# Optimization experiments

Hardware: AMD Instinct MI355X
Metric: run time of the kernel (lower is better)

## Reference

```python
import jax, jax.numpy as jnp
import numpy as np

B, T, F, G, H, N, C = 32, 64, 32, 32, 256, 20000, 32
EPS = 1e-5


def setup_inputs() -> dict:
    key = jax.random.key(0)
    ks = jax.random.split(key, 24)
    s = 0.05
    d = {}
    d["data_feats"] = jax.random.normal(ks[0], (B, T, F), jnp.float32)
    d["gat_output"] = jax.random.normal(ks[1], (B, N, G), jnp.float32)
    d["row_ids"] = jax.random.randint(ks[2], (B, T), 0, 2 * N, jnp.int32)
    d["node_ids"] = jax.random.randint(ks[3], (N,), 0, 2 * N, jnp.int32)
    # shared LSTM (2 layers): layer0 input F+G, layer1 input H; b = b_ih + b_hh fused
    d["shared_Wih0"] = jax.random.normal(ks[4], (4 * H, F + G)) * s
    d["shared_Whh0"] = jax.random.normal(ks[5], (4 * H, H)) * s
    d["shared_b0"] = jax.random.normal(ks[6], (4 * H,)) * s
    d["shared_Wih1"] = jax.random.normal(ks[7], (4 * H, H)) * s
    d["shared_Whh1"] = jax.random.normal(ks[8], (4 * H, H)) * s
    d["shared_b1"] = jax.random.normal(ks[9], (4 * H,)) * s
    # act/time/timeR LSTMs stacked on leading axis 3, each 2 layers of [4H,H]
    d["heads_Wih"] = jax.random.normal(ks[10], (3, 2, 4 * H, H)) * s
    d["heads_Whh"] = jax.random.normal(ks[11], (3, 2, 4 * H, H)) * s
    d["heads_b"] = jax.random.normal(ks[12], (3, 2, 4 * H)) * s
    d["bn_gnn_g"] = jnp.ones((G,), jnp.float32)
    d["bn_gnn_b"] = jnp.zeros((G,), jnp.float32)
    d["bn_shared_g"] = jnp.ones((H,), jnp.float32)
    d["bn_shared_b"] = jnp.zeros((H,), jnp.float32)
    d["heads_bn_g"] = jnp.ones((3, H), jnp.float32)
    d["heads_bn_b"] = jnp.zeros((3, H), jnp.float32)
    d["fc_act_W"] = jax.random.normal(ks[13], (C, H)) * s
    d["fc_act_b"] = jnp.zeros((C,), jnp.float32)
    d["fc_time_W"] = jax.random.normal(ks[14], (1, H)) * s
    d["fc_time_b"] = jnp.zeros((1,), jnp.float32)
    d["fc_timeR_W"] = jax.random.normal(ks[15], (1, H)) * s
    d["fc_timeR_b"] = jnp.zeros((1,), jnp.float32)
    return d


def batchnorm(x, gamma, beta):
    # BatchNorm1d training-mode: stats over (batch, length) per channel; x: [B, L, C]
    mean = jnp.mean(x, axis=(0, 1))
    var = jnp.var(x, axis=(0, 1))
    return (x - mean) * (gamma / jnp.sqrt(var + EPS)) + beta


def lstm_layer(x, Wih, Whh, b):
    # x: [B, T, Din]; PyTorch gate order i, f, g, o
    xp = jnp.einsum("btf,gf->btg", x, Wih) + b  # [B, T, 4H]
    h = Whh.shape[1]
    init = (jnp.zeros((x.shape[0], h), x.dtype), jnp.zeros((x.shape[0], h), x.dtype))

    def step(carry, xt):
        hprev, cprev = carry
        gates = xt + hprev @ Whh.T
        i, f, g, o = jnp.split(gates, 4, axis=-1)
        c = jax.nn.sigmoid(f) * cprev + jax.nn.sigmoid(i) * jnp.tanh(g)
        hnew = jax.nn.sigmoid(o) * jnp.tanh(c)
        return (hnew, c), hnew

    _, hs = jax.lax.scan(step, init, jnp.swapaxes(xp, 0, 1))
    return jnp.swapaxes(hs, 0, 1)  # [B, T, H]


def reference(data_feats, gat_output, row_ids, node_ids,
              shared_Wih0, shared_Whh0, shared_b0,
              shared_Wih1, shared_Whh1, shared_b1,
              heads_Wih, heads_Whh, heads_b,
              bn_gnn_g, bn_gnn_b, bn_shared_g, bn_shared_b,
              heads_bn_g, heads_bn_b,
              fc_act_W, fc_act_b, fc_time_W, fc_time_b, fc_timeR_W, fc_timeR_b):
    # --- graph branch: BN over GAT output, value-match lookup + gather ---
    gat_norm = batchnorm(gat_output, bn_gnn_g, bn_gnn_b)  # [B, N, G]
    eq = row_ids[:, :, None] == node_ids[None, None, :]   # [B, T, N]
    idx = jnp.argmax(eq, axis=-1)                          # first matching index
    found = jnp.any(eq, axis=-1)
    gathered = jnp.take_along_axis(gat_norm, idx[:, :, None], axis=1)  # [B, T, G]
    matched = jnp.where(found[:, :, None], gathered, 0.0)
    lstm_in = jnp.concatenate([data_feats, matched], axis=-1)  # [B, T, F+G]

    # --- shared 2-layer LSTM + BN (dropout off / eval) ---
    shared = lstm_layer(lstm_in, shared_Wih0, shared_Whh0, shared_b0)
    shared = lstm_layer(shared, shared_Wih1, shared_Whh1, shared_b1)
    shared = batchnorm(shared, bn_shared_g, bn_shared_b)

    # --- act / time / timeR head LSTMs (vmapped over the 3 heads) + BN ---
    def head(Wih, Whh, b, g, bb):
        hh = lstm_layer(shared, Wih[0], Whh[0], b[0])
        hh = lstm_layer(hh, Wih[1], Whh[1], b[1])
        return batchnorm(hh, g, bb)

    heads = jax.vmap(head)(heads_Wih, heads_Whh, heads_b, heads_bn_g, heads_bn_b)
    last = heads[:, :, -1, :]  # [3, B, H]

    act = jax.nn.softmax(last[0] @ fc_act_W.T + fc_act_b, axis=1)
    time = last[1] @ fc_time_W.T + fc_time_b
    timeR = last[2] @ fc_timeR_W.T + fc_timeR_b
    return act, time, timeR
```

## Files before the change

kernel.cpp:

```cpp
#include <hip/hip_runtime.h>
#include <hip/hip_fp16.h>
#include <math.h>

#define Bn 32
#define Tn 64
#define Fdim 32
#define Gdim 32
#define Hdim 256
#define Ndim 20000
#define Cdim 32
#define G4 1024
#define BT 2048
#define EPSc 1e-5f

__device__ __forceinline__ float sigmoidf_(float x){ return 1.0f/(1.0f + __expf(-x)); }
__device__ __forceinline__ float tanhf_(float x){ return 2.0f/(1.0f+__expf(-2.0f*x)) - 1.0f; }

typedef _Float16 h2t __attribute__((ext_vector_type(2)));

__device__ __forceinline__ float fdot2_(unsigned w, unsigned h, float acc){
#if defined(__has_builtin) && __has_builtin(__builtin_amdgcn_fdot2)
  return __builtin_amdgcn_fdot2(__builtin_bit_cast(h2t, w), __builtin_bit_cast(h2t, h), acc, false);
#else
  h2t a = __builtin_bit_cast(h2t, w), b = __builtin_bit_cast(h2t, h);
  acc = fmaf((float)a.x, (float)b.x, acc);
  return fmaf((float)a.y, (float)b.y, acc);
#endif
}

__global__ void init_kernel(float* ws){
  int i = blockIdx.x*256 + threadIdx.x;
  if (i < 2112) ws[i] = 0.0f;
  int* table = (int*)(ws + 2112);
  if (i < 40000) table[i] = 0x7fffffff;
}

__global__ void bn_stats_kernel(const float* __restrict__ gat, float* __restrict__ sums){
  __shared__ float ss[256], sq[256];
  int tid = threadIdx.x;
  int idx = blockIdx.x*256 + tid;
  int stride = gridDim.x*256;
  const int total = Bn*Ndim*Gdim;
  float s=0.f,q=0.f;
  for (int i=idx; i<total; i+=stride){ float v = gat[i]; s+=v; q+=v*v; }
  ss[tid]=s; sq[tid]=q; __syncthreads();
  for (int off=128; off>=32; off>>=1){
    if(tid<off){ ss[tid]+=ss[tid+off]; sq[tid]+=sq[tid+off]; }
    __syncthreads();
  }
  if (tid<32){ atomicAdd(&sums[tid], ss[tid]); atomicAdd(&sums[32+tid], sq[tid]); }
}

__global__ void table_kernel(const int* __restrict__ node_ids, int* __restrict__ table){
  int i = blockIdx.x*256 + threadIdx.x;
  if (i < Ndim) atomicMin(&table[node_ids[i]], i);
}

__global__ void build_input_kernel(const float* __restrict__ feats, const float* __restrict__ gat,
    const int* __restrict__ row_ids, const int* __restrict__ table, const float* __restrict__ sums,
    const float* __restrict__ bng, const float* __restrict__ bnb, float* __restrict__ out){
  int gt = blockIdx.x*256 + threadIdx.x;
  int pos = gt >> 6; int lane = gt & 63;
  float v;
  if (lane < 32){
    v = feats[pos*Fdim + lane];
  } else {
    int g = lane - 32;
    int r = row_ids[pos];
    int idx = table[r];
    if (idx < Ndim){
      int b = pos / Tn;
      float x = gat[(b*Ndim + idx)*Gdim + g];
      const float cnt = (float)(Bn*Ndim);
      float mean = sums[g]/cnt;
      float var  = sums[32+g]/cnt - mean*mean;
      v = (x-mean)*bng[g]*rsqrtf(var+EPSc) + bnb[g];
    } else v = 0.0f;
  }
  out[gt] = v;
}

struct TArgs { const float* src[8]; float* dst[8]; int K[8]; };
__global__ void transpose_kernel(TArgs a){
  __shared__ float tile[32][33];
  int mat = blockIdx.y;
  int K = a.K[mat];
  int tc = blockIdx.x & 7; int tr = blockIdx.x >> 3;
  if (tc*32 >= K) return;
  const float* src = a.src[mat]; float* dst = a.dst[mat];
  int tx = threadIdx.x; int ty = threadIdx.y;
  int r0 = tr*32, c0 = tc*32;
  #pragma unroll
  for (int i=0;i<4;i++){ int r = ty + i*8; tile[r][tx] = src[(r0+r)*K + c0+tx]; }
  __syncthreads();
  #pragma unroll
  for (int i=0;i<4;i++){ int r = ty + i*8; dst[(c0 + r)*G4 + r0 + tx] = tile[tx][r]; }
}

struct PkArgs { const float* src[8]; };
__global__ void pack_kernel(PkArgs a, unsigned* __restrict__ dst){
  int gid = blockIdx.x*256 + threadIdx.x;
  int m = gid >> 17;
  int rem = gid & 0x1FFFF;
  int q = rem & 3;
  int t2 = (rem >> 2) & 1023;
  int ci = rem >> 12;
  int c = ci >> 3, i = ci & 7;
  int j = t2 & 255, kq = t2 >> 8;
  int r = 4*j + c;
  int k = kq*64 + 8*i + 2*q;
  const float* W = a.src[m];
  float lo = W[r*256 + k], hi = W[r*256 + k + 1];
  unsigned ulo = (unsigned)__half_as_ushort(__float2half(lo));
  unsigned uhi = (unsigned)__half_as_ushort(__float2half(hi));
  dst[gid] = ulo | (uhi << 16);
}

struct PArgs { const float* x[3]; const float* wt[3]; const float* bias[3]; float* out[3]; int K; };
__global__ __launch_bounds__(256) void proj_kernel(PArgs a){
  int hd = blockIdx.z;
  int j  = blockIdx.y*256 + threadIdx.x;
  int m0 = blockIdx.x*4;
  const float* x  = a.x[hd];
  const float* wt = a.wt[hd];
  int K = a.K;
  float bv = a.bias[hd][j];
  float acc0=bv, acc1=bv, acc2=bv, acc3=bv;
  const float* x0 = x + m0*K;
  #pragma unroll 4
  for (int k=0;k<K;k++){
    float w = wt[k*G4 + j];
    acc0 = fmaf(x0[k],     w, acc0);
    acc1 = fmaf(x0[K+k],   w, acc1);
    acc2 = fmaf(x0[2*K+k], w, acc2);
    acc3 = fmaf(x0[3*K+k], w, acc3);
  }
  float* out = a.out[hd] + m0*G4 + j;
  out[0]=acc0; out[G4]=acc1; out[2*G4]=acc2; out[3*G4]=acc3;
}

struct RArgs { const float* xp[3]; const unsigned* wt[3]; float* out[3]; };
__global__ __launch_bounds__(1024,1) void rec_kernel(RArgs a){
  extern __shared__ float lds[];
  unsigned* lw   = (unsigned*)lds;
  float*    part = lds + 32768;
  unsigned* hp   = (unsigned*)(lds + 36864);
  int b = blockIdx.x, hd = blockIdx.y, tid = threadIdx.x;
  int j = tid & 255, kq = tid >> 8;
  const float* xp = a.xp[hd] + (size_t)b*Tn*G4;
  const unsigned* wt = a.wt[hd];
  float* out = a.out[hd] + (size_t)b*Tn*Hdim;

  unsigned w[96];
  #pragma unroll
  for (int c=0;c<4;c++){
    #pragma unroll
    for (int i=0;i<6;i++){
      uint4 v = *(const uint4*)(wt + ((c*8+i)*1024 + tid)*4);
      w[(c*6+i)*4+0]=v.x; w[(c*6+i)*4+1]=v.y; w[(c*6+i)*4+2]=v.z; w[(c*6+i)*4+3]=v.w;
    }
    #pragma unroll
    for (int i=6;i<8;i++){
      uint4 v = *(const uint4*)(wt + ((c*8+i)*1024 + tid)*4);
      *(uint4*)(lw + ((c*2+(i-6))*1024 + tid)*4) = v;
    }
  }
  float cst = 0.0f;
  if (tid < 128){ hp[tid] = 0u; hp[128+tid] = 0u; }
  __syncthreads();

  int p = 0;
  for (int t=0; t<Tn; t++){
    float ac0, ac1, ac2, ac3;
    if (kq == 0){
      float4 xv = *(const float4*)(xp + t*G4 + 4*j);
      ac0=xv.x; ac1=xv.y; ac2=xv.z; ac3=xv.w;
    } else { ac0=0.f; ac1=0.f; ac2=0.f; ac3=0.f; }
    const unsigned* hrow = hp + p*128 + kq*32;
    #pragma unroll
    for (int ic=0; ic<6; ic++){
      uint4 hv = *(const uint4*)(hrow + 4*ic);
      ac0=fdot2_(w[0*24+ic*4+0],hv.x,ac0); ac0=fdot2_(w[0*24+ic*4+1],hv.y,ac0);
      ac0=fdot2_(w[0*24+ic*4+2],hv.z,ac0); ac0=fdot2_(w[0*24+ic*4+3],hv.w,ac0);
      ac1=fdot2_(w[1*24+ic*4+0],hv.x,ac1); ac1=fdot2_(w[1*24+ic*4+1],hv.y,ac1);
      ac1=fdot2_(w[1*24+ic*4+2],hv.z,ac1); ac1=fdot2_(w[1*24+ic*4+3],hv.w,ac1);
      ac2=fdot2_(w[2*24+ic*4+0],hv.x,ac2); ac2=fdot2_(w[2*24+ic*4+1],hv.y,ac2);
      ac2=fdot2_(w[2*24+ic*4+2],hv.z,ac2); ac2=fdot2_(w[2*24+ic*4+3],hv.w,ac2);
      ac3=fdot2_(w[3*24+ic*4+0],hv.x,ac3); ac3=fdot2_(w[3*24+ic*4+1],hv.y,ac3);
      ac3=fdot2_(w[3*24+ic*4+2],hv.z,ac3); ac3=fdot2_(w[3*24+ic*4+3],hv.w,ac3);
    }
    #pragma unroll
    for (int ic=6; ic<8; ic++){
      uint4 hv = *(const uint4*)(hrow + 4*ic);
      { uint4 lv = *(const uint4*)(lw + ((0*2+(ic-6))*1024 + tid)*4);
        ac0=fdot2_(lv.x,hv.x,ac0); ac0=fdot2_(lv.y,hv.y,ac0);
        ac0=fdot2_(lv.z,hv.z,ac0); ac0=fdot2_(lv.w,hv.w,ac0); }
      { uint4 lv = *(const uint4*)(lw + ((1*2+(ic-6))*1024 + tid)*4);
        ac1=fdot2_(lv.x,hv.x,ac1); ac1=fdot2_(lv.y,hv.y,ac1);
        ac1=fdot2_(lv.z,hv.z,ac1); ac1=fdot2_(lv.w,hv.w,ac1); }
      { uint4 lv = *(const uint4*)(lw + ((2*2+(ic-6))*1024 + tid)*4);
        ac2=fdot2_(lv.x,hv.x,ac2); ac2=fdot2_(lv.y,hv.y,ac2);
        ac2=fdot2_(lv.z,hv.z,ac2); ac2=fdot2_(lv.w,hv.w,ac2); }
      { uint4 lv = *(const uint4*)(lw + ((3*2+(ic-6))*1024 + tid)*4);
        ac3=fdot2_(lv.x,hv.x,ac3); ac3=fdot2_(lv.y,hv.y,ac3);
        ac3=fdot2_(lv.z,hv.z,ac3); ac3=fdot2_(lv.w,hv.w,ac3); }
    }
    *(float4*)(part + kq*1024 + 4*j) = make_float4(ac0,ac1,ac2,ac3);
    __syncthreads();
    if (tid < 256){
      int u = tid;
      float gi = part[u]     + part[1024+u]     + part[2048+u]     + part[3072+u];
      float gf = part[256+u] + part[1024+256+u] + part[2048+256+u] + part[3072+256+u];
      float gg = part[512+u] + part[1024+512+u] + part[2048+512+u] + part[3072+512+u];
      float go = part[768+u] + part[1024+768+u] + part[2048+768+u] + part[3072+768+u];
      cst = sigmoidf_(gf)*cst + sigmoidf_(gi)*tanhf_(gg);
      float h = sigmoidf_(go)*tanhf_(cst);
      out[t*Hdim + u] = h;
      float hpartner = __shfl_xor(h, 1);
      if ((u & 1) == 0){
        unsigned ulo = (unsigned)__half_as_ushort(__float2half(h));
        unsigned uhi = (unsigned)__half_as_ushort(__float2half(hpartner));
        hp[(p^1)*128 + (u>>1)] = ulo | (uhi << 16);
      }
    }
    __syncthreads();
    p ^= 1;
  }
}

struct SArgs { const float* in[3]; float* stats[3]; };
__global__ void stats_kernel(SArgs a){
  int hd = blockIdx.y; int tid = threadIdx.x;
  const float* in = a.in[hd] + blockIdx.x*256*Hdim;
  float s=0.f,q=0.f;
  for (int r=0;r<256;r++){ float v = in[r*Hdim + tid]; s+=v; q+=v*v; }
  atomicAdd(&a.stats[hd][tid], s);
  atomicAdd(&a.stats[hd][Hdim+tid], q);
}

__global__ void norm_kernel(const float* __restrict__ in, const float* __restrict__ stats,
   const float* __restrict__ g, const float* __restrict__ bta, float* __restrict__ out){
  int i = blockIdx.x*256 + threadIdx.x;
  int h = i & 255;
  float mean = stats[h]*(1.0f/BT);
  float var  = stats[Hdim+h]*(1.0f/BT) - mean*mean;
  out[i] = (in[i]-mean)*g[h]*rsqrtf(var+EPSc) + bta[h];
}

__global__ __launch_bounds__(256) void final_kernel(
  const float* __restrict__ h0, const float* __restrict__ h1, const float* __restrict__ h2,
  const float* __restrict__ stats,
  const float* __restrict__ hbg, const float* __restrict__ hbb,
  const float* __restrict__ actW, const float* __restrict__ actB,
  const float* __restrict__ tW, const float* __restrict__ tB,
  const float* __restrict__ rW, const float* __restrict__ rB,
  float* __restrict__ outp){
  __shared__ float v0[Bn*Hdim];
  __shared__ float lg[Bn*Cdim];
  int tid = threadIdx.x;
  for (int i=tid; i<Bn*Hdim; i+=256){
    int b=i>>8, h=i&255;
    float sm = stats[512 + h], sq = stats[512+256+h];
    float mean = sm*(1.0f/BT); float var = sq*(1.0f/BT) - mean*mean;
    v0[i] = (h0[(b*Tn+63)*Hdim + h] - mean)*hbg[h]*rsqrtf(var+EPSc) + hbb[h];
  }
  __syncthreads();
  for (int i=tid; i<Bn*Cdim; i+=256){
    int b=i>>5, cc=i&31;
    float acc = actB[cc];
    const float* wrow = actW + cc*Hdim;
    const float* vrow = v0 + b*Hdim;
    #pragma unroll 4
    for (int h=0;h<Hdim;h++) acc = fmaf(vrow[h], wrow[h], acc);
    lg[i] = acc;
  }
  __syncthreads();
  if (tid < Bn){
    int b = tid;
    float m = -1e30f;
    #pragma unroll
    for (int cc=0; cc<Cdim; cc++) m = fmaxf(m, lg[b*Cdim+cc]);
    float e[Cdim]; float s = 0.f;
    #pragma unroll
    for (int cc=0; cc<Cdim; cc++){ float ee = __expf(lg[b*Cdim+cc]-m); e[cc]=ee; s+=ee; }
    float inv = 1.0f/s;
    #pragma unroll
    for (int cc=0; cc<Cdim; cc++) outp[b*Cdim+cc] = e[cc]*inv;
  }
  if (tid < 64){
    int b = tid & 31; int w = tid >> 5;
    const float* hh = w ? h2 : h1;
    const float* fw = w ? rW : tW;
    float fb = w ? rB[0] : tB[0];
    int hd = 1 + w;
    float acc = fb;
    for (int h=0; h<Hdim; h++){
      float sm = stats[(1+hd)*512 + h], sq = stats[(1+hd)*512+256+h];
      float mean = sm*(1.0f/BT); float var = sq*(1.0f/BT) - mean*mean;
      float v = (hh[(b*Tn+63)*Hdim + h] - mean)*hbg[hd*Hdim+h]*rsqrtf(var+EPSc) + hbb[hd*Hdim+h];
      acc = fmaf(v, fw[h], acc);
    }
    outp[1024 + w*32 + b] = acc;
  }
}

extern "C" void kernel_launch(void* const* d_in, const int* in_sizes, int n_in,
                              void* d_out, int out_size, void* d_ws, size_t ws_size,
                              hipStream_t stream){
  const float* data_feats = (const float*)d_in[0];
  const float* gat   = (const float*)d_in[1];
  const int*   row_ids  = (const int*)d_in[2];
  const int*   node_ids = (const int*)d_in[3];
  const float* sWih0 = (const float*)d_in[4];
  const float* sWhh0 = (const float*)d_in[5];
  const float* sb0   = (const float*)d_in[6];
  const float* sWih1 = (const float*)d_in[7];
  const float* sWhh1 = (const float*)d_in[8];
  const float* sb1   = (const float*)d_in[9];
  const float* hWih  = (const float*)d_in[10];
  const float* hWhh  = (const float*)d_in[11];
  const float* hb    = (const float*)d_in[12];
  const float* bng   = (const float*)d_in[13];
  const float* bnb   = (const float*)d_in[14];
  const float* bsg   = (const float*)d_in[15];
  const float* bsb   = (const float*)d_in[16];
  const float* hbg   = (const float*)d_in[17];
  const float* hbb   = (const float*)d_in[18];
  const float* actW  = (const float*)d_in[19];
  const float* actB  = (const float*)d_in[20];
  const float* tW    = (const float*)d_in[21];
  const float* tB    = (const float*)d_in[22];
  const float* rW    = (const float*)d_in[23];
  const float* rB    = (const float*)d_in[24];
  float* ws  = (float*)d_ws;
  float* out = (float*)d_out;

  const size_t S_GAT = 0;
  const size_t S_BN  = 64;
  const size_t TABLE = 2112;
  const size_t TWOFF = 42112;
  const size_t SLOT  = 262144;
  const size_t PKOFF = TWOFF + 8*SLOT;
  const size_t PSLOT = 131072;
  const size_t LSTM_IN = PKOFF + 8*PSLOT;
  const size_t XPOFF   = LSTM_IN + 131072;
  const size_t BUF0 = XPOFF + 3*2097152;
  const size_t BUF1 = BUF0 + 524288;
  const size_t BUFN = BUF1 + 524288;
  const size_t HB0  = BUFN + 524288;
  const size_t HB1  = HB0 + 3*524288;

  const int REC_LDS = 148480;
  hipFuncSetAttribute((const void*)rec_kernel, hipFuncAttributeMaxDynamicSharedMemorySize, REC_LDS);

  init_kernel<<<157,256,0,stream>>>(ws);
  bn_stats_kernel<<<2048,256,0,stream>>>(gat, ws+S_GAT);
  table_kernel<<<(Ndim+255)/256,256,0,stream>>>(node_ids, (int*)(ws+TABLE));
  build_input_kernel<<<512,256,0,stream>>>(data_feats, gat, row_ids, (int*)(ws+TABLE),
                                           ws+S_GAT, bng, bnb, ws+LSTM_IN);

  TArgs ta;
  float* tw = ws + TWOFF;
  ta.src[0]=sWih0; ta.K[0]=64;
  ta.src[1]=sWih1; ta.K[1]=256;
  for (int hd=0; hd<3; hd++) for (int l=0;l<2;l++){
    ta.src[2+hd*2+l] = hWih + (size_t)(hd*2+l)*G4*Hdim; ta.K[2+hd*2+l] = 256;
  }
  for (int i=0;i<8;i++) ta.dst[i] = tw + i*SLOT;
  transpose_kernel<<<dim3(256,8),dim3(32,8),0,stream>>>(ta);

  unsigned* pk = (unsigned*)(ws + PKOFF);
  PkArgs pka;
  pka.src[0]=sWhh0; pka.src[1]=sWhh1;
  for (int hd=0; hd<3; hd++) for (int l=0;l<2;l++)
    pka.src[2+hd*2+l] = hWhh + (size_t)(hd*2+l)*G4*Hdim;
  pack_kernel<<<4096,256,0,stream>>>(pka, pk);

  PArgs pa; RArgs ra; SArgs sa;
  pa.K=64; pa.x[0]=ws+LSTM_IN; pa.wt[0]=tw+0*SLOT; pa.bias[0]=sb0; pa.out[0]=ws+XPOFF;
  proj_kernel<<<dim3(512,4,1),256,0,stream>>>(pa);
  ra.xp[0]=ws+XPOFF; ra.wt[0]=pk+0*PSLOT; ra.out[0]=ws+BUF0;
  rec_kernel<<<dim3(32,1),1024,REC_LDS,stream>>>(ra);
  pa.K=256; pa.x[0]=ws+BUF0; pa.wt[0]=tw+1*SLOT; pa.bias[0]=sb1; pa.out[0]=ws+XPOFF;
  proj_kernel<<<dim3(512,4,1),256,0,stream>>>(pa);
  ra.xp[0]=ws+XPOFF; ra.wt[0]=pk+1*PSLOT; ra.out[0]=ws+BUF1;
  rec_kernel<<<dim3(32,1),1024,REC_LDS,stream>>>(ra);
  sa.in[0]=ws+BUF1; sa.stats[0]=ws+S_BN;
  stats_kernel<<<dim3(8,1),256,0,stream>>>(sa);
  norm_kernel<<<2048,256,0,stream>>>(ws+BUF1, ws+S_BN, bsg, bsb, ws+BUFN);
  pa.K=256;
  for (int hd=0;hd<3;hd++){
    pa.x[hd]=ws+BUFN; pa.wt[hd]=tw+(2+hd*2)*SLOT; pa.bias[hd]=hb + (size_t)(hd*2)*G4;
    pa.out[hd]=ws+XPOFF+(size_t)hd*2097152;
  }
  proj_kernel<<<dim3(512,4,3),256,0,stream>>>(pa);
  for (int hd=0;hd<3;hd++){
    ra.xp[hd]=ws+XPOFF+(size_t)hd*2097152; ra.wt[hd]=pk+(2+hd*2)*PSLOT; ra.out[hd]=ws+HB0+(size_t)hd*524288;
  }
  rec_kernel<<<dim3(32,3),1024,REC_LDS,stream>>>(ra);
  for (int hd=0;hd<3;hd++){
    pa.x[hd]=ws+HB0+(size_t)hd*524288; pa.wt[hd]=tw+(2+hd*2+1)*SLOT; pa.bias[hd]=hb + (size_t)(hd*2+1)*G4;
    pa.out[hd]=ws+XPOFF+(size_t)hd*2097152;
  }
  proj_kernel<<<dim3(512,4,3),256,0,stream>>>(pa);
  for (int hd=0;hd<3;hd++){
    ra.xp[hd]=ws+XPOFF+(size_t)hd*2097152; ra.wt[hd]=pk+(2+hd*2+1)*PSLOT; ra.out[hd]=ws+HB1+(size_t)hd*524288;
  }
  rec_kernel<<<dim3(32,3),1024,REC_LDS,stream>>>(ra);
  for (int hd=0;hd<3;hd++){ sa.in[hd]=ws+HB1+(size_t)hd*524288; sa.stats[hd]=ws+S_BN+(size_t)(1+hd)*512; }
  stats_kernel<<<dim3(8,3),256,0,stream>>>(sa);
  final_kernel<<<1,256,0,stream>>>(ws+HB1, ws+HB1+524288, ws+HB1+2*524288, ws+S_BN,
                                   hbg, hbb, actW, actB, tW, tB, rW, rB, out);
}
```

Baseline: 1.021 ms.

## Convert input projections to packed fp16 dot products with fp16 activations

Input-projection weights are now packed into fp16 pairs and transposed in one kernel. Layer inputs (the built LSTM input, the normalized shared output, and the recurrent outputs) are written as packed fp16 so the projection kernel can use fdot2 with 8 rows per thread instead of fp32 FMAs. The recurrent kernel also emits an fp16 copy of h for the next projection. This halves weight and activation traffic for the projections and doubles arithmetic per instruction, at the cost of fp16 rounding on activations and weights.

```diff
diff --git a/kernel.cpp b/kernel.cpp
--- a/kernel.cpp
+++ b/kernel.cpp
@@ -26,6 +26,12 @@
   acc = fmaf((float)a.x, (float)b.x, acc);
   return fmaf((float)a.y, (float)b.y, acc);
 #endif
+}
+
+__device__ __forceinline__ unsigned packh_(float lo, float hi){
+  unsigned ulo = (unsigned)__half_as_ushort(__float2half(lo));
+  unsigned uhi = (unsigned)__half_as_ushort(__float2half(hi));
+  return ulo | (uhi << 16);
 }
 
 __global__ void init_kernel(float* ws){
@@ -58,43 +64,56 @@
 
 __global__ void build_input_kernel(const float* __restrict__ feats, const float* __restrict__ gat,
     const int* __restrict__ row_ids, const int* __restrict__ table, const float* __restrict__ sums,
-    const float* __restrict__ bng, const float* __restrict__ bnb, float* __restrict__ out){
+    const float* __restrict__ bng, const float* __restrict__ bnb, unsigned* __restrict__ out){
   int gt = blockIdx.x*256 + threadIdx.x;
-  int pos = gt >> 6; int lane = gt & 63;
-  float v;
-  if (lane < 32){
-    v = feats[pos*Fdim + lane];
+  int pos = gt >> 5; int k2 = gt & 31;
+  float lo, hi;
+  if (k2 < 16){
+    float2 v = *(const float2*)(feats + pos*Fdim + 2*k2);
+    lo = v.x; hi = v.y;
   } else {
-    int g = lane - 32;
+    int g0 = 2*(k2-16);
     int r = row_ids[pos];
     int idx = table[r];
     if (idx < Ndim){
       int b = pos / Tn;
-      float x = gat[(b*Ndim + idx)*Gdim + g];
+      float2 x = *(const float2*)(gat + (size_t)(b*Ndim + idx)*Gdim + g0);
       const float cnt = (float)(Bn*Ndim);
-      float mean = sums[g]/cnt;
-      float var  = sums[32+g]/cnt - mean*mean;
-      v = (x-mean)*bng[g]*rsqrtf(var+EPSc) + bnb[g];
-    } else v = 0.0f;
-  }
-  out[gt] = v;
-}
-
-struct TArgs { const float* src[8]; float* dst[8]; int K[8]; };
-__global__ void transpose_kernel(TArgs a){
-  __shared__ float tile[32][33];
+      float m0 = sums[g0]/cnt,   v0 = sums[32+g0]/cnt - m0*m0;
+      float m1 = sums[g0+1]/cnt, v1 = sums[32+g0+1]/cnt - m1*m1;
+      lo = (x.x-m0)*bng[g0]*rsqrtf(v0+EPSc) + bnb[g0];
+      hi = (x.y-m1)*bng[g0+1]*rsqrtf(v1+EPSc) + bnb[g0+1];
+    } else { lo = 0.0f; hi = 0.0f; }
+  }
+  out[gt] = packh_(lo, hi);
+}
+
+struct TArgs { const float* src[8]; unsigned* dst[8]; int K[8]; };
+__global__ void packwih_kernel(TArgs a){
+  __shared__ unsigned tile[32][33];
   int mat = blockIdx.y;
   int K = a.K[mat];
-  int tc = blockIdx.x & 7; int tr = blockIdx.x >> 3;
-  if (tc*32 >= K) return;
-  const float* src = a.src[mat]; float* dst = a.dst[mat];
-  int tx = threadIdx.x; int ty = threadIdx.y;
-  int r0 = tr*32, c0 = tc*32;
+  int K2 = K >> 1;
+  int ktiles = K2 >> 5;
+  int tk = blockIdx.x & 3;
+  int tn = blockIdx.x >> 2;
+  if (tk >= ktiles) return;
+  const float* src = a.src[mat];
+  unsigned* dst = a.dst[mat];
+  int tx = threadIdx.x, ty = threadIdx.y;
+  int n0 = tn*32, k2_0 = tk*32;
   #pragma unroll
-  for (int i=0;i<4;i++){ int r = ty + i*8; tile[r][tx] = src[(r0+r)*K + c0+tx]; }
+  for (int i=0;i<4;i++){
+    int nn = ty + 8*i;
+    const float* p = src + (size_t)(n0+nn)*K + 2*(k2_0 + tx);
+    tile[nn][tx] = packh_(p[0], p[1]);
+  }
   __syncthreads();
   #pragma unroll
-  for (int i=0;i<4;i++){ int r = ty + i*8; dst[(c0 + r)*G4 + r0 + tx] = tile[tx][r]; }
+  for (int i=0;i<4;i++){
+    int r = ty + 8*i;
+    dst[(size_t)(k2_0 + r)*G4 + n0 + tx] = tile[tx][r];
+  }
 }
 
 struct PkArgs { const float* src[8]; };
@@ -110,36 +129,39 @@
   int r = 4*j + c;
   int k = kq*64 + 8*i + 2*q;
   const float* W = a.src[m];
-  float lo = W[r*256 + k], hi = W[r*256 + k + 1];
-  unsigned ulo = (unsigned)__half_as_ushort(__float2half(lo));
-  unsigned uhi = (unsigned)__half_as_ushort(__float2half(hi));
-  dst[gid] = ulo | (uhi << 16);
-}
-
-struct PArgs { const float* x[3]; const float* wt[3]; const float* bias[3]; float* out[3]; int K; };
+  dst[gid] = packh_(W[r*256 + k], W[r*256 + k + 1]);
+}
+
+struct PArgs { const unsigned* x[3]; const unsigned* wt[3]; const float* bias[3]; float* out[3]; int K2; };
 __global__ __launch_bounds__(256) void proj_kernel(PArgs a){
   int hd = blockIdx.z;
-  int j  = blockIdx.y*256 + threadIdx.x;
-  int m0 = blockIdx.x*4;
-  const float* x  = a.x[hd];
-  const float* wt = a.wt[hd];
-  int K = a.K;
-  float bv = a.bias[hd][j];
-  float acc0=bv, acc1=bv, acc2=bv, acc3=bv;
-  const float* x0 = x + m0*K;
-  #pragma unroll 4
-  for (int k=0;k<K;k++){
-    float w = wt[k*G4 + j];
-    acc0 = fmaf(x0[k],     w, acc0);
-    acc1 = fmaf(x0[K+k],   w, acc1);
-    acc2 = fmaf(x0[2*K+k], w, acc2);
-    acc3 = fmaf(x0[3*K+k], w, acc3);
-  }
-  float* out = a.out[hd] + m0*G4 + j;
-  out[0]=acc0; out[G4]=acc1; out[2*G4]=acc2; out[3*G4]=acc3;
-}
-
-struct RArgs { const float* xp[3]; const unsigned* wt[3]; float* out[3]; };
+  int n  = blockIdx.y*256 + threadIdx.x;
+  int m0 = blockIdx.x*8;
+  int K2 = a.K2;
+  const unsigned* xh = a.x[hd] + (size_t)m0*K2;
+  const unsigned* wt = a.wt[hd];
+  float bv = a.bias[hd][n];
+  float acc[8];
+  #pragma unroll
+  for (int i=0;i<8;i++) acc[i]=bv;
+  for (int k2=0;k2<K2;k2+=4){
+    unsigned w0 = wt[(size_t)(k2+0)*G4+n];
+    unsigned w1 = wt[(size_t)(k2+1)*G4+n];
+    unsigned w2 = wt[(size_t)(k2+2)*G4+n];
+    unsigned w3 = wt[(size_t)(k2+3)*G4+n];
+    #pragma unroll
+    for (int i=0;i<8;i++){
+      uint4 xv = *(const uint4*)(xh + i*K2 + k2);
+      acc[i]=fdot2_(w0,xv.x,acc[i]); acc[i]=fdot2_(w1,xv.y,acc[i]);
+      acc[i]=fdot2_(w2,xv.z,acc[i]); acc[i]=fdot2_(w3,xv.w,acc[i]);
+    }
+  }
+  float* out = a.out[hd] + (size_t)m0*G4 + n;
+  #pragma unroll
+  for (int i=0;i<8;i++) out[i*G4]=acc[i];
+}
+
+struct RArgs { const float* xp[3]; const unsigned* wt[3]; float* out[3]; unsigned* outh[3]; };
 __global__ __launch_bounds__(1024,1) void rec_kernel(RArgs a){
   extern __shared__ float lds[];
   unsigned* lw   = (unsigned*)lds;
@@ -150,6 +172,7 @@
   const float* xp = a.xp[hd] + (size_t)b*Tn*G4;
   const unsigned* wt = a.wt[hd];
   float* out = a.out[hd] + (size_t)b*Tn*Hdim;
+  unsigned* outh = a.outh[hd] + (size_t)b*Tn*128;
 
   unsigned w[96];
   #pragma unroll
@@ -218,9 +241,9 @@
       out[t*Hdim + u] = h;
       float hpartner = __shfl_xor(h, 1);
       if ((u & 1) == 0){
-        unsigned ulo = (unsigned)__half_as_ushort(__float2half(h));
-        unsigned uhi = (unsigned)__half_as_ushort(__float2half(hpartner));
-        hp[(p^1)*128 + (u>>1)] = ulo | (uhi << 16);
+        unsigned hh = packh_(h, hpartner);
+        hp[(p^1)*128 + (u>>1)] = hh;
+        outh[t*128 + (u>>1)] = hh;
       }
     }
     __syncthreads();
@@ -239,12 +262,16 @@
 }
 
 __global__ void norm_kernel(const float* __restrict__ in, const float* __restrict__ stats,
-   const float* __restrict__ g, const float* __restrict__ bta, float* __restrict__ out){
-  int i = blockIdx.x*256 + threadIdx.x;
-  int h = i & 255;
-  float mean = stats[h]*(1.0f/BT);
-  float var  = stats[Hdim+h]*(1.0f/BT) - mean*mean;
-  out[i] = (in[i]-mean)*g[h]*rsqrtf(var+EPSc) + bta[h];
+   const float* __restrict__ g, const float* __restrict__ bta, unsigned* __restrict__ outh){
+  int i2 = blockIdx.x*256 + threadIdx.x;
+  int h2 = i2 & 127; int m = i2 >> 7;
+  int h0 = 2*h2;
+  float2 v = *(const float2*)(in + (size_t)m*Hdim + h0);
+  float m0 = stats[h0]*(1.0f/BT),   v0 = stats[Hdim+h0]*(1.0f/BT) - m0*m0;
+  float m1 = stats[h0+1]*(1.0f/BT), v1 = stats[Hdim+h0+1]*(1.0f/BT) - m1*m1;
+  float lo = (v.x-m0)*g[h0]*rsqrtf(v0+EPSc) + bta[h0];
+  float hi = (v.y-m1)*g[h0+1]*rsqrtf(v1+EPSc) + bta[h0+1];
+  outh[i2] = packh_(lo, hi);
 }
 
 __global__ __launch_bounds__(256) void final_kernel(
@@ -338,17 +365,16 @@
   const size_t S_GAT = 0;
   const size_t S_BN  = 64;
   const size_t TABLE = 2112;
-  const size_t TWOFF = 42112;
-  const size_t SLOT  = 262144;
-  const size_t PKOFF = TWOFF + 8*SLOT;
+  const size_t WIHP  = 42112;
   const size_t PSLOT = 131072;
-  const size_t LSTM_IN = PKOFF + 8*PSLOT;
-  const size_t XPOFF   = LSTM_IN + 131072;
-  const size_t BUF0 = XPOFF + 3*2097152;
-  const size_t BUF1 = BUF0 + 524288;
-  const size_t BUFN = BUF1 + 524288;
-  const size_t HB0  = BUFN + 524288;
-  const size_t HB1  = HB0 + 3*524288;
+  const size_t WHHP  = WIHP + 8*PSLOT;
+  const size_t LSTM_INH = WHHP + 8*PSLOT;
+  const size_t XPOFF = LSTM_INH + 65536;
+  const size_t BUF0H = XPOFF + 3*2097152;
+  const size_t BUF1  = BUF0H + 262144;
+  const size_t BUFNH = BUF1 + 524288;
+  const size_t HB0H  = BUFNH + 262144;
+  const size_t HB1   = HB0H + 3*262144;
 
   const int REC_LDS = 148480;
   hipFuncSetAttribute((const void*)rec_kernel, hipFuncAttributeMaxDynamicSharedMemorySize, REC_LDS);
@@ -356,55 +382,58 @@
   init_kernel<<<157,256,0,stream>>>(ws);
   bn_stats_kernel<<<2048,256,0,stream>>>(gat, ws+S_GAT);
   table_kernel<<<(Ndim+255)/256,256,0,stream>>>(node_ids, (int*)(ws+TABLE));
-  build_input_kernel<<<512,256,0,stream>>>(data_feats, gat, row_ids, (int*)(ws+TABLE),
-                                           ws+S_GAT, bng, bnb, ws+LSTM_IN);
-
+  build_input_kernel<<<256,256,0,stream>>>(data_feats, gat, row_ids, (int*)(ws+TABLE),
+                                           ws+S_GAT, bng, bnb, (unsigned*)(ws+LSTM_INH));
+
+  unsigned* wih = (unsigned*)(ws + WIHP);
   TArgs ta;
-  float* tw = ws + TWOFF;
   ta.src[0]=sWih0; ta.K[0]=64;
   ta.src[1]=sWih1; ta.K[1]=256;
   for (int hd=0; hd<3; hd++) for (int l=0;l<2;l++){
     ta.src[2+hd*2+l] = hWih + (size_t)(hd*2+l)*G4*Hdim; ta.K[2+hd*2+l] = 256;
   }
-  for (int i=0;i<8;i++) ta.dst[i] = tw + i*SLOT;
-  transpose_kernel<<<dim3(256,8),dim3(32,8),0,stream>>>(ta);
-
-  unsigned* pk = (unsigned*)(ws + PKOFF);
+  for (int i=0;i<8;i++) ta.dst[i] = wih + (size_t)i*PSLOT;
+  packwih_kernel<<<dim3(128,8),dim3(32,8),0,stream>>>(ta);
+
+  unsigned* whh = (unsigned*)(ws + WHHP);
   PkArgs pka;
   pka.src[0]=sWhh0; pka.src[1]=sWhh1;
   for (int hd=0; hd<3; hd++) for (int l=0;l<2;l++)
     pka.src[2+hd*2+l] = hWhh + (size_t)(hd*2+l)*G4*Hdim;
-  pack_kernel<<<4096,256,0,stream>>>(pka, pk);
+  pack_kernel<<<4096,256,0,stream>>>(pka, whh);
 
   PArgs pa; RArgs ra; SArgs sa;
-  pa.K=64; pa.x[0]=ws+LSTM_IN; pa.wt[0]=tw+0*SLOT; pa.bias[0]=sb0; pa.out[0]=ws+XPOFF;
-  proj_kernel<<<dim3(512,4,1),256,0,stream>>>(pa);
-  ra.xp[0]=ws+XPOFF; ra.wt[0]=pk+0*PSLOT; ra.out[0]=ws+BUF0;
+  pa.K2=32; pa.x[0]=(unsigned*)(ws+LSTM_INH); pa.wt[0]=wih+0*PSLOT; pa.bias[0]=sb0; pa.out[0]=ws+XPOFF;
+  proj_kernel<<<dim3(256,4,1),256,0,stream>>>(pa);
+  ra.xp[0]=ws+XPOFF; ra.wt[0]=whh+0*PSLOT; ra.out[0]=ws+BUF1;  ra.outh[0]=(unsigned*)(ws+BUF0H);
   rec_kernel<<<dim3(32,1),1024,REC_LDS,stream>>>(ra);
-  pa.K=256; pa.x[0]=ws+BUF0; pa.wt[0]=tw+1*SLOT; pa.bias[0]=sb1; pa.out[0]=ws+XPOFF;
-  proj_kernel<<<dim3(512,4,1),256,0,stream>>>(pa);
-  ra.xp[0]=ws+XPOFF; ra.wt[0]=pk+1*PSLOT; ra.out[0]=ws+BUF1;
+  pa.K2=128; pa.x[0]=(unsigned*)(ws+BUF0H); pa.wt[0]=wih+1*PSLOT; pa.bias[0]=sb1; pa.out[0]=ws+XPOFF;
+  proj_kernel<<<dim3(256,4,1),256,0,stream>>>(pa);
+  ra.xp[0]=ws+XPOFF; ra.wt[0]=whh+1*PSLOT; ra.out[0]=ws+BUF1; ra.outh[0]=(unsigned*)(ws+BUF0H);
   rec_kernel<<<dim3(32,1),1024,REC_LDS,stream>>>(ra);
   sa.in[0]=ws+BUF1; sa.stats[0]=ws+S_BN;
   stats_kernel<<<dim3(8,1),256,0,stream>>>(sa);
-  norm_kernel<<<2048,256,0,stream>>>(ws+BUF1, ws+S_BN, bsg, bsb, ws+BUFN);
-  pa.K=256;
+  norm_kernel<<<1024,256,0,stream>>>(ws+BUF1, ws+S_BN, bsg, bsb, (unsigned*)(ws+BUFNH));
+  pa.K2=128;
   for (int hd=0;hd<3;hd++){
-    pa.x[hd]=ws+BUFN; pa.wt[hd]=tw+(2+hd*2)*SLOT; pa.bias[hd]=hb + (size_t)(hd*2)*G4;
+    pa.x[hd]=(unsigned*)(ws+BUFNH); pa.wt[hd]=wih+(size_t)(2+hd*2)*PSLOT; pa.bias[hd]=hb + (size_t)(hd*2)*G4;
     pa.out[hd]=ws+XPOFF+(size_t)hd*2097152;
   }
-  proj_kernel<<<dim3(512,4,3),256,0,stream>>>(pa);
+  proj_kernel<<<dim3(256,4,3),256,0,stream>>>(pa);
   for (int hd=0;hd<3;hd++){
-    ra.xp[hd]=ws+XPOFF+(size_t)hd*2097152; ra.wt[hd]=pk+(2+hd*2)*PSLOT; ra.out[hd]=ws+HB0+(size_t)hd*524288;
+    ra.xp[hd]=ws+XPOFF+(size_t)hd*2097152; ra.wt[hd]=whh+(size_t)(2+hd*2)*PSLOT;
+    ra.out[hd]=ws+HB1+(size_t)hd*524288;  ra.outh[hd]=(unsigned*)(ws+HB0H)+(size_t)hd*262144;
   }
   rec_kernel<<<dim3(32,3),1024,REC_LDS,stream>>>(ra);
   for (int hd=0;hd<3;hd++){
-    pa.x[hd]=ws+HB0+(size_t)hd*524288; pa.wt[hd]=tw+(2+hd*2+1)*SLOT; pa.bias[hd]=hb + (size_t)(hd*2+1)*G4;
+    pa.x[hd]=(unsigned*)(ws+HB0H)+(size_t)hd*262144; pa.wt[hd]=wih+(size_t)(2+hd*2+1)*PSLOT;
+    pa.bias[hd]=hb + (size_t)(hd*2+1)*G4;
     pa.out[hd]=ws+XPOFF+(size_t)hd*2097152;
   }
-  proj_kernel<<<dim3(512,4,3),256,0,stream>>>(pa);
+  proj_kernel<<<dim3(256,4,3),256,0,stream>>>(pa);
   for (int hd=0;hd<3;hd++){
-    ra.xp[hd]=ws+XPOFF+(size_t)hd*2097152; ra.wt[hd]=pk+(2+hd*2+1)*PSLOT; ra.out[hd]=ws+HB1+(size_t)hd*524288;
+    ra.xp[hd]=ws+XPOFF+(size_t)hd*2097152; ra.wt[hd]=whh+(size_t)(2+hd*2+1)*PSLOT;
+    ra.out[hd]=ws+HB1+(size_t)hd*524288; ra.outh[hd]=(unsigned*)(ws+HB0H)+(size_t)hd*262144;
   }
   rec_kernel<<<dim3(32,3),1024,REC_LDS,stream>>>(ra);
   for (int hd=0;hd<3;hd++){ sa.in[hd]=ws+HB1+(size_t)hd*524288; sa.stats[hd]=ws+S_BN+(size_t)(1+hd)*512; }
```

Result: faster. 869.5 us (-14.8%).
